# Performance work log

Hardware: AMD Instinct MI355X
Metric: run time of the kernel (lower is better)

Reference implementation:

```python
import jax, jax.numpy as jnp
import numpy as np
from jax import lax

EPS = 1e-5
F_CH = 32  # TIM future channels = int(256/8)
B_CH = 32  # TIM past channels (note: source bug -> these are zeroed, not shifted)


def inorm(x):
    # InstanceNorm3d (no affine): normalize each (b, c) over (T, H, W), biased var
    m = jnp.mean(x, axis=(2, 3, 4), keepdims=True)
    v = jnp.var(x, axis=(2, 3, 4), keepdims=True)
    return (x - m) * lax.rsqrt(v + EPS)


def conv1x1(x, w):
    # pointwise conv: x [B,C,T,H,W], w [O,C]
    return jnp.einsum('bcthw,oc->bothw', x, w)


def dwconv(x, w, pad):
    # depthwise 3D conv; w [C,1,kd,kh,kw], pad = [(pd,pd),(ph,ph),(pw,pw)]
    return lax.conv_general_dilated(
        x, w, window_strides=(1, 1, 1), padding=pad,
        feature_group_count=x.shape[1],
        dimension_numbers=('NCDHW', 'OIDHW', 'NCDHW'))


def tim(x):
    # Non-circular temporal interlacing. Faithful to source (past slice is a no-op):
    # channels [0:f]  <- x shifted from future (t+1), zero-padded at last frame
    # channels [f:f+b] <- zeros
    # channels [f+b:] <- identity
    f, b = F_CH, B_CH
    fut = jnp.concatenate([x[:, :f, 1:], jnp.zeros_like(x[:, :f, :1])], axis=2)
    mid = jnp.zeros_like(x[:, f:f + b])
    return jnp.concatenate([fut, mid, x[:, f + b:]], axis=1)


def setup_inputs() -> dict:
    key = jax.random.key(0)
    ks = jax.random.split(key, 7)
    cin, hid, cout = 64, 256, 64
    x = jax.random.normal(ks[0], (4, cin, 16, 64, 64), dtype=jnp.float32)
    w1 = jax.random.normal(ks[1], (hid, cin), dtype=jnp.float32) * 0.05
    w_dw_s = jax.random.normal(ks[2], (hid, 1, 1, 3, 3), dtype=jnp.float32) * 0.1
    w_dw_t = jax.random.normal(ks[3], (hid, 1, 3, 1, 1), dtype=jnp.float32) * 0.1
    w_se1 = jax.random.normal(ks[4], (hid // 4, hid), dtype=jnp.float32) * 0.05
    w_se2 = jax.random.normal(ks[5], (hid, hid // 4), dtype=jnp.float32) * 0.05
    w_proj = jax.random.normal(ks[6], (cout, hid), dtype=jnp.float32) * 0.05
    return {'x': x, 'w1': w1, 'w_dw_s': w_dw_s, 'w_dw_t': w_dw_t,
            'w_se1': w_se1, 'w_se2': w_se2, 'w_proj': w_proj}


def reference(x, w1, w_dw_s, w_dw_t, w_se1, w_se2, w_proj):
    shortcut = x
    # stage1: expand 1x1 conv + IN + ReLU
    h = jax.nn.relu(inorm(conv1x1(x, w1)))
    # temporal interlace (zero-FLOP channel shift)
    h = tim(h)
    # stage2: depthwise spatial (1,3,3) + IN + ReLU
    h = jax.nn.relu(inorm(dwconv(h, w_dw_s, [(0, 0), (1, 1), (1, 1)])))
    # stage3: depthwise temporal (3,1,1) + IN + ReLU
    h = jax.nn.relu(inorm(dwconv(h, w_dw_t, [(1, 1), (0, 0), (0, 0)])))
    # squeeze-excite
    y = jnp.mean(h, axis=(2, 3, 4), keepdims=True)           # [B,C,1,1,1]
    y = jax.nn.relu(jnp.einsum('bcthw,oc->bothw', y, w_se1))
    y = jax.nn.sigmoid(jnp.einsum('bcthw,oc->bothw', y, w_se2))
    h = h * y
    # proj 1x1 + IN, residual, maxpool (1,2,2)
    out = inorm(conv1x1(h, w_proj)) + shortcut
    out = lax.reduce_window(out, -jnp.inf, lax.max,
                            (1, 1, 1, 2, 2), (1, 1, 1, 2, 2), 'VALID')
    return out
```

## Files before the change

### kernel.cpp

```cpp
#include <hip/hip_runtime.h>
#include <hip/hip_bf16.h>

#define B_   4
#define CIN  64
#define HID  256
#define COUT 64
#define T_   16
#define H_   64
#define W_   64
#define HW_  (H_*W_)
#define THW  (T_*HW_)
#define EPS  1e-5f

typedef unsigned short ushort_t;
typedef unsigned int   uint_t;
typedef short bf16x8 __attribute__((ext_vector_type(8)));
typedef float f32x4  __attribute__((ext_vector_type(4)));

#define SM1   0
#define SIS1  1024
#define SM2   2048
#define SIS2  3072
#define SM3   4096
#define SIS3  5120
#define SSES  6144
#define SAL   7168
#define SBE   8192
__device__ float g_stats[10240];
__device__ float g_p2s[16384], g_p2ss[16384];
__device__ float g_p1s[1048576], g_p1ss[1048576];
__device__ ushort_t g_wpack[32768];

__device__ __forceinline__ float bf2f(ushort_t u) {
    return __uint_as_float(((uint_t)u) << 16);
}
__device__ __forceinline__ ushort_t f2bf(float f) {
    uint_t u = __float_as_uint(f);
    uint_t r = u + 0x7fffu + ((u >> 16) & 1u);
    return (ushort_t)(r >> 16);
}
__device__ __forceinline__ void loadnorm8(const ushort_t* p, float a, float bb,
                                          float* v) {
    uint4 u = *(const uint4*)p;
    uint_t uu[4] = {u.x, u.y, u.z, u.w};
    #pragma unroll
    for (int j = 0; j < 4; ++j) {
        v[2*j]   = fmaxf(fmaf(__uint_as_float(uu[j] << 16),         a, bb), 0.f);
        v[2*j+1] = fmaxf(fmaf(__uint_as_float(uu[j] & 0xffff0000u), a, bb), 0.f);
    }
}

__global__ __launch_bounds__(256) void k_prep(const float* __restrict__ w1,
                                              const float* __restrict__ wproj) {
    int idx = blockIdx.x*256 + threadIdx.x;
    {
        int j = idx & 7, lane = (idx>>3) & 63, ot = (idx>>9) & 3;
        int ks = (idx>>11) & 1, wv = idx >> 12;
        int ln = lane & 15, q = lane >> 4;
        int o = wv*64 + ot*16 + ln, k = ks*32 + q*8 + j;
        g_wpack[idx] = f2bf(w1[o*CIN + k]);
    }
    {
        int j = idx & 7, lane = (idx>>3) & 63, ot = (idx>>9) & 3, kg = idx >> 11;
        int ln = lane & 15, q = lane >> 4;
        int o = ot*16 + ln, k = kg*32 + q*8 + j;
        g_wpack[16384 + idx] = f2bf(wproj[o*HID + k]);
    }
}

__global__ __launch_bounds__(256) void k_expand(const float* __restrict__ x,
                                                ushort_t* __restrict__ h1, int b0) {
    __shared__ ushort_t Bs[64*72];
    const int tid = threadIdx.x;
    const int bx  = blockIdx.x;
    const int bb  = blockIdx.y, gb = b0 + bb;
    const int pos0 = bx * 64;
    const int lane = tid & 63, wv = tid >> 6;
    const int q = lane >> 4, ln = lane & 15;

    bf16x8 af[2][4];
    #pragma unroll
    for (int ks = 0; ks < 2; ++ks)
        #pragma unroll
        for (int ot = 0; ot < 4; ++ot)
            af[ks][ot] = *(const bf16x8*)&g_wpack[(((wv*2+ks)*4+ot)<<9) + lane*8];

    #pragma unroll
    for (int i = 0; i < 4; ++i) {
        int lin = i*1024 + tid*4;
        int k = lin >> 6, n0 = lin & 63;
        float4 v = *(const float4*)&x[(size_t)(gb*CIN + k) * THW + pos0 + n0];
        ushort_t* d = &Bs[k*72 + ((n0 + 16*((k>>3)&3)) & 63)];
        d[0] = f2bf(v.x); d[1] = f2bf(v.y); d[2] = f2bf(v.z); d[3] = f2bf(v.w);
    }
    __syncthreads();

    f32x4 acc[4][4];
    #pragma unroll
    for (int i = 0; i < 4; ++i)
        #pragma unroll
        for (int j = 0; j < 4; ++j)
            acc[i][j] = (f32x4){0.f,0.f,0.f,0.f};

    #pragma unroll
    for (int ks = 0; ks < 2; ++ks) {
        bf16x8 bfr[4];
        #pragma unroll
        for (int nt = 0; nt < 4; ++nt) {
            union { short s[8]; bf16x8 v; } bu;
            #pragma unroll
            for (int j = 0; j < 8; ++j) {
                int k = ks*32 + q*8 + j;
                int nn = (nt*16 + ln + 16*((k>>3)&3)) & 63;
                bu.s[j] = (short)Bs[k*72 + nn];
            }
            bfr[nt] = bu.v;
        }
        #pragma unroll
        for (int ot = 0; ot < 4; ++ot)
            #pragma unroll
            for (int nt = 0; nt < 4; ++nt)
                acc[ot][nt] = __builtin_amdgcn_mfma_f32_16x16x32_bf16(
                    af[ks][ot], bfr[nt], acc[ot][nt], 0, 0, 0);
    }

    const int pbase = ((bb*1024 + bx) << 8);
    #pragma unroll
    for (int ot = 0; ot < 4; ++ot) {
        float sr[4]  = {0.f,0.f,0.f,0.f};
        float ssr[4] = {0.f,0.f,0.f,0.f};
        #pragma unroll
        for (int nt = 0; nt < 4; ++nt)
            #pragma unroll
            for (int r = 0; r < 4; ++r) {
                int o = wv*64 + ot*16 + q*4 + r;
                int n = nt*16 + ln;
                ushort_t us = f2bf(acc[ot][nt][r]);
                h1[((size_t)bb*HID + o)*THW + pos0 + n] = us;
                float v = bf2f(us);
                sr[r] += v; ssr[r] = fmaf(v, v, ssr[r]);
            }
        #pragma unroll
        for (int r = 0; r < 4; ++r) {
            float s = sr[r], ss = ssr[r];
            #pragma unroll
            for (int m = 1; m < 16; m <<= 1) {
                s  += __shfl_xor(s,  m);
                ss += __shfl_xor(ss, m);
            }
            if (ln == 0) {
                int o = wv*64 + ot*16 + q*4 + r;
                g_p1s [pbase + o] = s;
                g_p1ss[pbase + o] = ss;
            }
        }
    }
}

__global__ __launch_bounds__(256) void k_fin1() {
    const int bc = blockIdx.x;
    const int bb = bc >> 8, o = bc & 255;
    const int tid = threadIdx.x;
    float s = 0.f, ss = 0.f;
    #pragma unroll
    for (int i = 0; i < 4; ++i) {
        int bx = i*256 + tid;
        int base = ((bb*1024 + bx) << 8) + o;
        s += g_p1s[base]; ss += g_p1ss[base];
    }
    #pragma unroll
    for (int m = 32; m > 0; m >>= 1) {
        s  += __shfl_xor(s,  m);
        ss += __shfl_xor(ss, m);
    }
    __shared__ float ls[4], lss[4];
    int wid = tid >> 6, lane = tid & 63;
    if (lane == 0) { ls[wid] = s; lss[wid] = ss; }
    __syncthreads();
    if (tid == 0) {
        float st  = ls[0]+ls[1]+ls[2]+ls[3];
        float sst = lss[0]+lss[1]+lss[2]+lss[3];
        float m = st * (1.f/THW);
        float v = sst * (1.f/THW) - m*m;
        g_stats[SM1  + bc] = m;
        g_stats[SIS1 + bc] = 1.f / sqrtf(v + EPS);
    }
}

__global__ __launch_bounds__(256) void k_proj(const ushort_t* __restrict__ h3,
                                              float* __restrict__ proj) {
    __shared__ ushort_t Bs[64*136];
    const int tid = threadIdx.x;
    const int bb  = blockIdx.y;
    const int pos0 = blockIdx.x * 128;
    const int lane = tid & 63, wv = tid >> 6;
    const int q = lane >> 4, ln = lane & 15;

    f32x4 acc[4][2];
    #pragma unroll
    for (int i = 0; i < 4; ++i) {
        acc[i][0] = (f32x4){0.f,0.f,0.f,0.f};
        acc[i][1] = (f32x4){0.f,0.f,0.f,0.f};
    }

    for (int kc = 0; kc < 4; ++kc) {
        #pragma unroll
        for (int i = 0; i < 8; ++i) {
            int lin = i*1024 + tid*4;
            int kl = lin >> 7, n0 = lin & 127;
            int ch = bb*HID + kc*64 + kl;
            float al = g_stats[SAL + ch], be = g_stats[SBE + ch];
            ushort_t* d = &Bs[kl*136 + ((n0 + 16*((kl>>3)&7)) & 127)];
            if (al == 0.f) {
                d[0] = 0; d[1] = 0; d[2] = 0; d[3] = 0;
            } else {
                uint2 u = *(const uint2*)&h3[(size_t)ch * THW + pos0 + n0];
                float f0 = __uint_as_float(u.x << 16);
                float f1 = __uint_as_float(u.x & 0xffff0000u);
                float f2 = __uint_as_float(u.y << 16);
                float f3 = __uint_as_float(u.y & 0xffff0000u);
                d[0] = f2bf(fmaxf(fmaf(f0, al, be), 0.f));
                d[1] = f2bf(fmaxf(fmaf(f1, al, be), 0.f));
                d[2] = f2bf(fmaxf(fmaf(f2, al, be), 0.f));
                d[3] = f2bf(fmaxf(fmaf(f3, al, be), 0.f));
            }
        }
        __syncthreads();

        #pragma unroll
        for (int ks = 0; ks < 2; ++ks) {
            int kg = kc*2 + ks;
            bf16x8 af[4];
            #pragma unroll
            for (int ot = 0; ot < 4; ++ot)
                af[ot] = *(const bf16x8*)&g_wpack[16384 + ((kg*4+ot)<<9) + lane*8];
            bf16x8 bfr[2];
            #pragma unroll
            for (int nt = 0; nt < 2; ++nt) {
                union { short s[8]; bf16x8 v; } bu;
                #pragma unroll
                for (int j = 0; j < 8; ++j) {
                    int kl = ks*32 + q*8 + j;
                    int nn = (wv*32 + nt*16 + ln + 16*((kl>>3)&7)) & 127;
                    bu.s[j] = (short)Bs[kl*136 + nn];
                }
                bfr[nt] = bu.v;
            }
            #pragma unroll
            for (int ot = 0; ot < 4; ++ot)
                #pragma unroll
                for (int nt = 0; nt < 2; ++nt)
                    acc[ot][nt] = __builtin_amdgcn_mfma_f32_16x16x32_bf16(
                        af[ot], bfr[nt], acc[ot][nt], 0, 0, 0);
        }
        __syncthreads();
    }

    #pragma unroll
    for (int ot = 0; ot < 4; ++ot)
        #pragma unroll
        for (int nt = 0; nt < 2; ++nt)
            #pragma unroll
            for (int r = 0; r < 4; ++r) {
                int o = ot*16 + q*4 + r;
                int n = wv*32 + nt*16 + ln;
                proj[((size_t)bb*COUT + o)*THW + pos0 + n] = acc[ot][nt][r];
            }
}

__global__ __launch_bounds__(256) void k_dws(const ushort_t* __restrict__ h1,
                                             const float* __restrict__ wdw,
                                             ushort_t* __restrict__ h2) {
    const int tid = threadIdx.x;
    const int t   = blockIdx.x;
    const int bc  = blockIdx.y;
    const int o   = bc & (HID-1);
    const int pidx = bc*16 + t;

    const bool zeroall = (o >= 32 && o < 64);
    const bool zerot   = (o < 32 && t == T_-1);
    if (zeroall || zerot) {
        if (tid == 0) { g_p2s[pidx] = 0.f; g_p2ss[pidx] = 0.f; }
        return;
    }
    const int ts = (o < 32) ? t + 1 : t;
    const float a  = g_stats[SIS1 + bc];
    const float bb = -g_stats[SM1 + bc] * a;
    const ushort_t* sp = h1 + (size_t)bc * THW + ts*HW_;
    ushort_t*       op = h2 + (size_t)bc * THW + t*HW_;

    __shared__ float pl[64*66];
    #pragma unroll
    for (int j = 0; j < 2; ++j) {
        int lin = j*2048 + tid*8;
        int y = lin >> 6, xx = lin & 63;
        float v[8];
        loadnorm8(sp + lin, a, bb, v);
        float* dst = &pl[y*66 + xx];
        #pragma unroll
        for (int i = 0; i < 8; ++i) dst[i] = v[i];
    }
    __syncthreads();

    float wf[9];
    #pragma unroll
    for (int k = 0; k < 9; ++k) wf[k] = wdw[o*9 + k];

    float s = 0.f, ss = 0.f;
    #pragma unroll
    for (int g = 0; g < 2; ++g) {
        int lin = g*2048 + tid*8;
        int y = lin >> 6, x0 = lin & 63;
        float v[3][10];
        #pragma unroll
        for (int dy = 0; dy < 3; ++dy) {
            int yy = y + dy - 1;
            if (yy < 0 || yy >= H_) {
                #pragma unroll
                for (int j = 0; j < 10; ++j) v[dy][j] = 0.f;
            } else {
                const float* rp = &pl[yy*66];
                v[dy][0] = (x0 == 0)  ? 0.f : rp[x0-1];
                #pragma unroll
                for (int i = 0; i < 8; ++i) v[dy][1+i] = rp[x0+i];
                v[dy][9] = (x0 == 56) ? 0.f : rp[x0+8];
            }
        }
        uint_t outp[4];
        #pragma unroll
        for (int i2 = 0; i2 < 4; ++i2) {
            float o0 = 0.f, o1 = 0.f;
            #pragma unroll
            for (int dy = 0; dy < 3; ++dy)
                #pragma unroll
                for (int dx = 0; dx < 3; ++dx) {
                    float w = wf[dy*3+dx];
                    o0 = fmaf(w, v[dy][2*i2 + dx],     o0);
                    o1 = fmaf(w, v[dy][2*i2 + 1 + dx], o1);
                }
            ushort_t u0 = f2bf(o0), u1 = f2bf(o1);
            float r0 = bf2f(u0), r1 = bf2f(u1);
            s += r0 + r1; ss = fmaf(r0, r0, fmaf(r1, r1, ss));
            outp[i2] = (uint_t)u0 | ((uint_t)u1 << 16);
        }
        uint4 r; r.x = outp[0]; r.y = outp[1]; r.z = outp[2]; r.w = outp[3];
        *(uint4*)(op + lin) = r;
    }

    #pragma unroll
    for (int m = 32; m > 0; m >>= 1) {
        s  += __shfl_xor(s,  m);
        ss += __shfl_xor(ss, m);
    }
    __shared__ float ls[4], lss[4];
    int wid = tid >> 6, lane = tid & 63;
    if (lane == 0) { ls[wid] = s; lss[wid] = ss; }
    __syncthreads();
    if (tid == 0) {
        g_p2s[pidx]  = ls[0]+ls[1]+ls[2]+ls[3];
        g_p2ss[pidx] = lss[0]+lss[1]+lss[2]+lss[3];
    }
}

__global__ __launch_bounds__(512) void k_dwt(const ushort_t* __restrict__ h2,
                                             const float* __restrict__ wdt,
                                             ushort_t* __restrict__ h3) {
    const int tid = threadIdx.x;
    const int bc  = blockIdx.x;
    const int o   = bc & (HID-1);
    __shared__ float ls[8], lss[8];
    __shared__ float sa, sb;
    int wid = tid >> 6, lane = tid & 63;

    if (o >= 32 && o < 64) {
        if (tid == 0) {
            g_stats[SM3  + bc] = 0.f;
            g_stats[SIS3 + bc] = 1.f / sqrtf(EPS);
            g_stats[SSES + bc] = 0.f;
        }
        return;
    }

    {
        float ps  = (tid < 16) ? g_p2s [bc*16 + tid] : 0.f;
        float pss = (tid < 16) ? g_p2ss[bc*16 + tid] : 0.f;
        #pragma unroll
        for (int m = 8; m > 0; m >>= 1) {
            ps  += __shfl_xor(ps,  m);
            pss += __shfl_xor(pss, m);
        }
        if (tid == 0) {
            float m = ps * (1.f/THW);
            float v = pss * (1.f/THW) - m*m;
            float is = 1.f / sqrtf(v + EPS);
            g_stats[SM2  + bc] = m;
            g_stats[SIS2 + bc] = is;
            sa = is; sb = -m * is;
        }
    }
    __syncthreads();
    const float a = sa, bb = sb;
    const bool last_invalid = (o < 32);
    const float znorm = fmaxf(bb, 0.f);
    const float w0 = wdt[o*3+0], w1 = wdt[o*3+1], w2 = wdt[o*3+2];
    const int pos = tid * 8;
    const ushort_t* sp = h2 + (size_t)bc * THW + pos;
    ushort_t*       op = h3 + (size_t)bc * THW + pos;

    float p[8], c[8], n[8];
    #pragma unroll
    for (int i = 0; i < 8; ++i) p[i] = 0.f;
    loadnorm8(sp,       a, bb, c);
    loadnorm8(sp + HW_, a, bb, n);

    float s = 0.f, ss = 0.f;
    #pragma unroll
    for (int t = 0; t < T_; ++t) {
        uint_t outp[4];
        #pragma unroll
        for (int i2 = 0; i2 < 4; ++i2) {
            float o0 = fmaf(w0, p[2*i2],   fmaf(w1, c[2*i2],   w2 * n[2*i2]));
            float o1 = fmaf(w0, p[2*i2+1], fmaf(w1, c[2*i2+1], w2 * n[2*i2+1]));
            ushort_t u0 = f2bf(o0), u1 = f2bf(o1);
            float r0 = bf2f(u0), r1 = bf2f(u1);
            s += r0 + r1; ss = fmaf(r0, r0, fmaf(r1, r1, ss));
            outp[i2] = (uint_t)u0 | ((uint_t)u1 << 16);
        }
        uint4 r; r.x = outp[0]; r.y = outp[1]; r.z = outp[2]; r.w = outp[3];
        *(uint4*)(op + t*HW_) = r;

        #pragma unroll
        for (int i = 0; i < 8; ++i) { p[i] = c[i]; c[i] = n[i]; }
        if (t + 2 < T_) {
            if (last_invalid && t + 2 == T_-1) {
                #pragma unroll
                for (int i = 0; i < 8; ++i) n[i] = znorm;
            } else {
                loadnorm8(sp + (t+2)*HW_, a, bb, n);
            }
        } else {
            #pragma unroll
            for (int i = 0; i < 8; ++i) n[i] = 0.f;
        }
    }

    #pragma unroll
    for (int m = 32; m > 0; m >>= 1) {
        s  += __shfl_xor(s,  m);
        ss += __shfl_xor(ss, m);
    }
    if (lane == 0) { ls[wid] = s; lss[wid] = ss; }
    __syncthreads();
    if (tid == 0) {
        float st = 0.f, sst = 0.f;
        #pragma unroll
        for (int i = 0; i < 8; ++i) { st += ls[i]; sst += lss[i]; }
        float m = st * (1.f/THW);
        float v = sst * (1.f/THW) - m*m;
        float is = 1.f / sqrtf(v + EPS);
        g_stats[SM3  + bc] = m;
        g_stats[SIS3 + bc] = is;
        sa = is; sb = -m * is;
    }
    __syncthreads();

    const float a3 = sa, b3 = sb;
    float s2 = 0.f;
    #pragma unroll
    for (int t = 0; t < T_; ++t) {
        uint4 u = *(const uint4*)(op + t*HW_);
        uint_t uu[4] = {u.x, u.y, u.z, u.w};
        #pragma unroll
        for (int j = 0; j < 4; ++j) {
            s2 += fmaxf(fmaf(__uint_as_float(uu[j] << 16),         a3, b3), 0.f);
            s2 += fmaxf(fmaf(__uint_as_float(uu[j] & 0xffff0000u), a3, b3), 0.f);
        }
    }
    #pragma unroll
    for (int m = 32; m > 0; m >>= 1) s2 += __shfl_xor(s2, m);
    if (lane == 0) ls[wid] = s2;
    __syncthreads();
    if (tid == 0) {
        float st = 0.f;
        #pragma unroll
        for (int i = 0; i < 8; ++i) st += ls[i];
        g_stats[SSES + bc] = st * (1.f/THW);
    }
}

__global__ __launch_bounds__(256) void k_semlp(const float* __restrict__ wse1,
                                               const float* __restrict__ wse2) {
    __shared__ float mv[HID];
    __shared__ float y1[64];
    const int bb = blockIdx.x, tid = threadIdx.x;
    mv[tid] = g_stats[SSES + bb*HID + tid];
    __syncthreads();
    if (tid < 64) {
        float acc = 0.f;
        #pragma unroll 8
        for (int c = 0; c < HID; ++c) acc = fmaf(wse1[tid*HID + c], mv[c], acc);
        y1[tid] = fmaxf(acc, 0.f);
    }
    __syncthreads();
    float z = 0.f;
    #pragma unroll
    for (int c = 0; c < 64; ++c) z = fmaf(wse2[tid*64 + c], y1[c], z);
    float se = 1.f / (1.f + expf(-z));
    const int bc = bb*HID + tid;
    float al = g_stats[SIS3 + bc] * se;
    if (tid >= 32 && tid < 64) al = 0.f;
    g_stats[SAL + bc] = al;
    g_stats[SBE + bc] = -g_stats[SM3 + bc] * al;
}

__global__ __launch_bounds__(1024) void k_final(const float* __restrict__ proj,
                                                const float* __restrict__ x,
                                                float* __restrict__ out, int b0) {
    const int bo  = blockIdx.x;
    const int tid = threadIdx.x;
    const float* p = proj + (size_t)bo * THW;

    float s = 0.f, ss = 0.f;
    #pragma unroll
    for (int i = 0; i < THW/(1024*4); ++i) {
        float4 u = *(const float4*)(p + i*4096 + tid*4);
        s += u.x; ss = fmaf(u.x, u.x, ss);
        s += u.y; ss = fmaf(u.y, u.y, ss);
        s += u.z; ss = fmaf(u.z, u.z, ss);
        s += u.w; ss = fmaf(u.w, u.w, ss);
    }
    #pragma unroll
    for (int off = 32; off > 0; off >>= 1) {
        s  += __shfl_down(s,  off, 64);
        ss += __shfl_down(ss, off, 64);
    }
    __shared__ float ls[16], lss[16];
    __shared__ float sa, sb;
    int wid = tid >> 6, lane = tid & 63;
    if (lane == 0) { ls[wid] = s; lss[wid] = ss; }
    __syncthreads();
    if (tid == 0) {
        float st = 0.f, sst = 0.f;
        #pragma unroll
        for (int i = 0; i < 16; ++i) { st += ls[i]; sst += lss[i]; }
        float m = st * (1.f/THW);
        float v = sst * (1.f/THW) - m*m;
        float is = 1.f / sqrtf(v + EPS);
        sa = is; sb = -m * is;
    }
    __syncthreads();
    const float a = sa, bb = sb;

    const size_t gbase = (size_t)(b0*COUT + bo) * THW;
    float* op = out + (size_t)(b0*COUT + bo) * (T_*1024);
    #pragma unroll
    for (int i = 0; i < 16; ++i) {
        int idx = i*1024 + tid;
        int xx = idx & 31, yy = (idx >> 5) & 31, t = idx >> 10;
        float m = -3.4e38f;
        #pragma unroll
        for (int r = 0; r < 2; ++r) {
            size_t off = (size_t)t*HW_ + (size_t)(2*yy + r)*W_ + 2*xx;
            float2 p2 = *(const float2*)(p + off);
            float2 x2 = *(const float2*)(x + gbase + off);
            float v0 = fmaf(p2.x, a, bb) + x2.x;
            float v1 = fmaf(p2.y, a, bb) + x2.y;
            m = fmaxf(m, fmaxf(v0, v1));
        }
        op[idx] = m;
    }
}

extern "C" void kernel_launch(void* const* d_in, const int* in_sizes, int n_in,
                              void* d_out, int out_size, void* d_ws, size_t ws_size,
                              hipStream_t stream) {
    const float* x     = (const float*)d_in[0];
    const float* w1    = (const float*)d_in[1];
    const float* wdws  = (const float*)d_in[2];
    const float* wdwt  = (const float*)d_in[3];
    const float* wse1  = (const float*)d_in[4];
    const float* wse2  = (const float*)d_in[5];
    const float* wproj = (const float*)d_in[6];
    float* out = (float*)d_out;

    const size_t perb = 2ull * HID * THW * sizeof(ushort_t);
    int nb = (ws_size >= 4*perb) ? 4 : (ws_size >= 2*perb) ? 2 : 1;

    k_prep<<<64, 256, 0, stream>>>(w1, wproj);

    for (int b0 = 0; b0 < B_; b0 += nb) {
        char* ws = (char*)d_ws;
        ushort_t* h1   = (ushort_t*)ws;
        ushort_t* h2   = (ushort_t*)(ws + (size_t)nb * HID*THW*2);
        ushort_t* h3   = h1;
        float*    proj = (float*)h2;

        k_expand<<<dim3(THW/64, nb), 256, 0, stream>>>(x, h1, b0);
        k_fin1  <<<nb*HID, 256, 0, stream>>>();
        k_dws   <<<dim3(T_, nb*HID), 256, 0, stream>>>(h1, wdws, h2);
        k_dwt   <<<nb*HID, 512, 0, stream>>>(h2, wdwt, h3);
        k_semlp <<<nb, 256, 0, stream>>>(wse1, wse2);
        k_proj  <<<dim3(THW/128, nb), 256, 0, stream>>>(h3, proj);
        k_final <<<nb*COUT, 1024, 0, stream>>>(proj, x, out, b0);
    }
}
```

Before: 383.1 us.

## Fuse projection stats into proj GEMM epilogue and keep dwt outputs in registers

The projection kernel now reduces per-channel sum and sum-of-squares for each 128-position tile and writes partials, so the final kernel reads 512 partials instead of rescanning the whole fp32 projection tensor for InstanceNorm stats. Stage-1 partial stats are relaid out channel-major for contiguous reads in the finalize kernel. The temporal depthwise kernel keeps its 16 output vectors in registers for the SE mean pass rather than reloading them from global memory. This trades extra registers and a shared-memory reduction for less global traffic.

```diff
diff --git a/kernel.cpp b/kernel.cpp
--- a/kernel.cpp
+++ b/kernel.cpp
@@ -29,6 +29,7 @@
 __device__ float g_stats[10240];
 __device__ float g_p2s[16384], g_p2ss[16384];
 __device__ float g_p1s[1048576], g_p1ss[1048576];
+__device__ float g_pps[131072], g_ppss[131072];
 __device__ ushort_t g_wpack[32768];
 
 __device__ __forceinline__ float bf2f(ushort_t u) {
@@ -124,7 +125,6 @@
                     af[ks][ot], bfr[nt], acc[ot][nt], 0, 0, 0);
     }
 
-    const int pbase = ((bb*1024 + bx) << 8);
     #pragma unroll
     for (int ot = 0; ot < 4; ++ot) {
         float sr[4]  = {0.f,0.f,0.f,0.f};
@@ -149,9 +149,9 @@
                 ss += __shfl_xor(ss, m);
             }
             if (ln == 0) {
-                int o = wv*64 + ot*16 + q*4 + r;
-                g_p1s [pbase + o] = s;
-                g_p1ss[pbase + o] = ss;
+                int ch = bb*HID + wv*64 + ot*16 + q*4 + r;
+                g_p1s [ch*1024 + bx] = s;
+                g_p1ss[ch*1024 + bx] = ss;
             }
         }
     }
@@ -159,14 +159,12 @@
 
 __global__ __launch_bounds__(256) void k_fin1() {
     const int bc = blockIdx.x;
-    const int bb = bc >> 8, o = bc & 255;
     const int tid = threadIdx.x;
     float s = 0.f, ss = 0.f;
     #pragma unroll
     for (int i = 0; i < 4; ++i) {
         int bx = i*256 + tid;
-        int base = ((bb*1024 + bx) << 8) + o;
-        s += g_p1s[base]; ss += g_p1ss[base];
+        s += g_p1s[bc*1024 + bx]; ss += g_p1ss[bc*1024 + bx];
     }
     #pragma unroll
     for (int m = 32; m > 0; m >>= 1) {
@@ -190,9 +188,11 @@
 __global__ __launch_bounds__(256) void k_proj(const ushort_t* __restrict__ h3,
                                               float* __restrict__ proj) {
     __shared__ ushort_t Bs[64*136];
+    __shared__ float sred[4][64], ssred[4][64];
     const int tid = threadIdx.x;
+    const int bx  = blockIdx.x;
     const int bb  = blockIdx.y;
-    const int pos0 = blockIdx.x * 128;
+    const int pos0 = bx * 128;
     const int lane = tid & 63, wv = tid >> 6;
     const int q = lane >> 4, ln = lane & 15;
 
@@ -259,13 +259,34 @@
     #pragma unroll
     for (int ot = 0; ot < 4; ++ot)
         #pragma unroll
-        for (int nt = 0; nt < 2; ++nt)
-            #pragma unroll
-            for (int r = 0; r < 4; ++r) {
+        for (int r = 0; r < 4; ++r) {
+            float v0 = acc[ot][0][r], v1 = acc[ot][1][r];
+            {
                 int o = ot*16 + q*4 + r;
-                int n = wv*32 + nt*16 + ln;
-                proj[((size_t)bb*COUT + o)*THW + pos0 + n] = acc[ot][nt][r];
-            }
+                int n0 = wv*32 + ln;
+                proj[((size_t)bb*COUT + o)*THW + pos0 + n0]      = v0;
+                proj[((size_t)bb*COUT + o)*THW + pos0 + n0 + 16] = v1;
+            }
+            float s = v0 + v1;
+            float ss = fmaf(v0, v0, v1*v1);
+            #pragma unroll
+            for (int m = 1; m < 16; m <<= 1) {
+                s  += __shfl_xor(s,  m);
+                ss += __shfl_xor(ss, m);
+            }
+            if (ln == 0) {
+                int o = ot*16 + q*4 + r;
+                sred[wv][o] = s; ssred[wv][o] = ss;
+            }
+        }
+    __syncthreads();
+    if (tid < 64) {
+        float s  = sred[0][tid] + sred[1][tid] + sred[2][tid] + sred[3][tid];
+        float ss = ssred[0][tid] + ssred[1][tid] + ssred[2][tid] + ssred[3][tid];
+        int ch = bb*COUT + tid;
+        g_pps [ch*512 + bx] = s;
+        g_ppss[ch*512 + bx] = ss;
+    }
 }
 
 __global__ __launch_bounds__(256) void k_dws(const ushort_t* __restrict__ h1,
@@ -413,6 +434,7 @@
     loadnorm8(sp,       a, bb, c);
     loadnorm8(sp + HW_, a, bb, n);
 
+    uint4 keep[16];
     float s = 0.f, ss = 0.f;
     #pragma unroll
     for (int t = 0; t < T_; ++t) {
@@ -427,6 +449,7 @@
             outp[i2] = (uint_t)u0 | ((uint_t)u1 << 16);
         }
         uint4 r; r.x = outp[0]; r.y = outp[1]; r.z = outp[2]; r.w = outp[3];
+        keep[t] = r;
         *(uint4*)(op + t*HW_) = r;
 
         #pragma unroll
@@ -468,8 +491,7 @@
     float s2 = 0.f;
     #pragma unroll
     for (int t = 0; t < T_; ++t) {
-        uint4 u = *(const uint4*)(op + t*HW_);
-        uint_t uu[4] = {u.x, u.y, u.z, u.w};
+        uint_t uu[4] = {keep[t].x, keep[t].y, keep[t].z, keep[t].w};
         #pragma unroll
         for (int j = 0; j < 4; ++j) {
             s2 += fmaxf(fmaf(__uint_as_float(uu[j] << 16),         a3, b3), 0.f);
@@ -521,13 +543,9 @@
     const float* p = proj + (size_t)bo * THW;
 
     float s = 0.f, ss = 0.f;
-    #pragma unroll
-    for (int i = 0; i < THW/(1024*4); ++i) {
-        float4 u = *(const float4*)(p + i*4096 + tid*4);
-        s += u.x; ss = fmaf(u.x, u.x, ss);
-        s += u.y; ss = fmaf(u.y, u.y, ss);
-        s += u.z; ss = fmaf(u.z, u.z, ss);
-        s += u.w; ss = fmaf(u.w, u.w, ss);
+    if (tid < 512) {
+        s  = g_pps [bo*512 + tid];
+        ss = g_ppss[bo*512 + tid];
     }
     #pragma unroll
     for (int off = 32; off > 0; off >>= 1) {
@@ -542,7 +560,7 @@
     if (tid == 0) {
         float st = 0.f, sst = 0.f;
         #pragma unroll
-        for (int i = 0; i < 16; ++i) { st += ls[i]; sst += lss[i]; }
+        for (int i = 0; i < 8; ++i) { st += ls[i]; sst += lss[i]; }
         float m = st * (1.f/THW);
         float v = sst * (1.f/THW) - m*m;
         float is = 1.f / sqrtf(v + EPS);
```

Measured after the change: 383.6 us. Within noise of the previous version (+0.1%).
